# Optimization experiments

Measured on AMD Instinct MI355X. Metric: run time of the kernel, lower is better.

The kernel has to match this reference:

```python
import jax, jax.numpy as jnp
import numpy as np

# dims: T=tgt len, B=batch, S=src len, E=n_embed, H=n_hidden, V=vocab, L=n_layers
T, B, S, E, H, V, L = 64, 64, 256, 512, 1024, 16000, 2
PAD, SOS, EOS, COPY = 0, 1, 2, 3
EPS = 1e-7
NEG = -1e9  # additive mask for padded source positions


def setup_inputs() -> dict:
    key = jax.random.key(0)
    ks = jax.random.split(key, 16)
    r = lambda i, shape, s=0.02: jax.random.normal(ks[i], shape, jnp.float32) * s
    return dict(
        ref_tokens=jax.random.randint(ks[0], (T, B), 0, V),
        att_tokens=jax.random.randint(ks[1], (S, B), 0, V),
        att_features=jax.random.normal(ks[2], (S, B, H), jnp.float32),
        h0=jnp.zeros((L, B, H), jnp.float32),
        c0=jnp.zeros((L, B, H), jnp.float32),
        embed_w=r(3, (V, E)).at[PAD].set(0.0),  # padding_idx row zeroed
        W_ih0=r(4, (4 * H, E + H)), W_hh0=r(5, (4 * H, H)),
        b_ih0=r(6, (4 * H,), 0.01), b_hh0=r(7, (4 * H,), 0.01),
        W_ih1=r(8, (4 * H, H)), W_hh1=r(9, (4 * H, H)),
        b_ih1=r(10, (4 * H,), 0.01), b_hh1=r(11, (4 * H,), 0.01),
        Wk=r(12, (H, H)), bk=jnp.zeros(H, jnp.float32),
        Wq=r(13, (H, H)), bq=jnp.zeros(H, jnp.float32),
        Wc=r(14, (H, 2 * H)), bc=jnp.zeros(H, jnp.float32),
        Wp=r(15, (V, H)), bp=jnp.zeros(V, jnp.float32),
        Wsp=jax.random.normal(jax.random.fold_in(key, 99), (1, H), jnp.float32) * 0.02,
        bsp=jnp.zeros(1, jnp.float32),
    )


def _lstm_cell(x, h, c, W_ih, W_hh, b_ih, b_hh):
    # PyTorch gate order: i, f, g, o
    g = x @ W_ih.T + b_ih + h @ W_hh.T + b_hh
    i, f, gg, o = jnp.split(g, 4, axis=1)
    cn = jax.nn.sigmoid(f) * c + jax.nn.sigmoid(i) * jnp.tanh(gg)
    hn = jax.nn.sigmoid(o) * jnp.tanh(cn)
    return hn, cn


def reference(ref_tokens, att_tokens, att_features, h0, c0, embed_w,
              W_ih0, W_hh0, b_ih0, b_hh0, W_ih1, W_hh1, b_ih1, b_hh1,
              Wk, bk, Wq, bq, Wc, bc, Wp, bp, Wsp, bsp):
    mask = (att_tokens == PAD).astype(jnp.float32)              # (S,B)
    keys = jnp.einsum('sbh,kh->sbk', att_features, Wk) + bk     # (S,B,H), step-invariant
    bidx = jnp.broadcast_to(jnp.arange(B), (S, B))

    def step(carry, tok_t):
        feed, h, c = carry
        emb = embed_w[tok_t]                                    # (B,E)
        x = jnp.concatenate([emb, feed], axis=1)                # (B,E+H) concat_feed
        h0n, c0n = _lstm_cell(x, h[0], c[0], W_ih0, W_hh0, b_ih0, b_hh0)
        h1n, c1n = _lstm_cell(h0n, h[1], c[1], W_ih1, W_hh1, b_ih1, b_hh1)
        hidden = h1n                                            # (B,H) top layer
        # SimpleAttention: dot-product over time axis
        query = hidden @ Wq.T + bq
        scores = jnp.einsum('sbh,bh->sb', keys, query) + mask * NEG
        dist = jax.nn.softmax(scores, axis=0)                   # (S,B)
        summary = jnp.einsum('sb,sbh->bh', dist, att_features)
        comb = jnp.concatenate([hidden, summary], axis=1) @ Wc.T + bc  # (B,H)
        logits = comb @ Wp.T + bp                               # (B,V)
        probs = jax.nn.softmax(logits, axis=1)
        seq_probs = jax.nn.softmax(hidden @ Wsp.T + bsp, axis=1)  # (B,1) == 1 (single attn)
        wdist = dist * seq_probs[:, 0][None, :] * probs[:, COPY][None, :]  # (S,B)
        # one-hot projection matmul == scatter-add of weighted dist into token bins
        copy_probs = jnp.zeros((B, V), jnp.float32).at[bidx, att_tokens].add(wdist) + EPS
        comb_p = (copy_probs + probs).at[:, COPY].set(0.0)
        pred_logits = jnp.log(comb_p)                           # (B,V)
        return (comb, jnp.stack([h0n, h1n]), jnp.stack([c0n, c1n])), pred_logits

    feed0 = jnp.zeros((B, H), jnp.float32)
    _, preds = jax.lax.scan(step, (feed0, h0, c0), ref_tokens)
    return preds  # (T,B,V)
```

## Files before the change

kernel.cpp:

```cpp
#include <hip/hip_runtime.h>
#include <stdint.h>
#include <math.h>

#define Td 64
#define Bd 64
#define Sd 256
#define Ed 512
#define Hd 1024
#define Vd 16000
#define G4 4096

typedef short v8s __attribute__((ext_vector_type(8)));
typedef float v4f __attribute__((ext_vector_type(4)));

__device__ __forceinline__ float b2f(unsigned short v) {
  union { unsigned int u; float f; } x; x.u = ((unsigned int)v) << 16; return x.f;
}
__device__ __forceinline__ unsigned short f2b(float f) {
  union { float f; unsigned int u; } x; x.f = f;
  unsigned int u = x.u + 0x7fffu + ((x.u >> 16) & 1u);
  return (unsigned short)(u >> 16);
}


__global__ __launch_bounds__(256) void k_f2b(const float* __restrict__ s,
                                             unsigned short* __restrict__ d, int n) {
  int i = blockIdx.x * 256 + threadIdx.x;
  if (i < n) d[i] = f2b(s[i]);
}

__global__ __launch_bounds__(256) void k_cvtgate(const float* __restrict__ ih,
                                                 const float* __restrict__ hh,
                                                 unsigned short* __restrict__ dst,
                                                 int Kih, int Ktot) {
  int i = blockIdx.x * 256 + threadIdx.x;
  int np = i / Ktot;
  int k = i - np * Ktot;
  int n = ((np & 3) << 10) + (np >> 2);
  float v = (k < Kih) ? ih[(size_t)n * Kih + k]
                      : hh[(size_t)n * (Ktot - Kih) + (k - Kih)];
  dst[i] = f2b(v);
}

__global__ __launch_bounds__(256) void k_embed(const int* __restrict__ tok,
                                               const float* __restrict__ ew,
                                               unsigned short* __restrict__ dst) {
  int i = blockIdx.x * 256 + threadIdx.x;
  int e = i & (Ed - 1);
  int tb = i >> 9;
  dst[i] = f2b(ew[(size_t)tok[tb] * Ed + e]);
}

__global__ __launch_bounds__(256) void k_mt(const float* __restrict__ Wk,
                                            const float* __restrict__ Wq,
                                            unsigned short* __restrict__ MTT) {
  __shared__ float sk[32][33], sq[32][33];
  int tx = threadIdx.x & 15, ty = threadIdx.x >> 4;
  int n0 = blockIdx.x * 32, k0 = blockIdx.y * 32;
  float a00 = 0, a01 = 0, a10 = 0, a11 = 0;
  for (int jc = 0; jc < 32; jc++) {
    __syncthreads();
    for (int i = threadIdx.x; i < 1024; i += 256) {
      int r = i >> 5, c = i & 31;
      sk[r][c] = Wk[(jc * 32 + r) * Hd + n0 + c];
      sq[r][c] = Wq[(jc * 32 + r) * Hd + k0 + c];
    }
    __syncthreads();
    for (int j = 0; j < 32; j++) {
      float kv0 = sk[j][tx], kv1 = sk[j][tx + 16];
      float qv0 = sq[j][ty], qv1 = sq[j][ty + 16];
      a00 += kv0 * qv0; a01 += kv0 * qv1; a10 += kv1 * qv0; a11 += kv1 * qv1;
    }
  }
  MTT[(k0 + ty) * Hd + n0 + tx]             = f2b(a00);
  MTT[(k0 + ty + 16) * Hd + n0 + tx]        = f2b(a01);
  MTT[(k0 + ty) * Hd + n0 + tx + 16]        = f2b(a10);
  MTT[(k0 + ty + 16) * Hd + n0 + tx + 16]   = f2b(a11);
}

__global__ __launch_bounds__(256) void k_biasq(const float* __restrict__ bq,
                                               const float* __restrict__ Wk,
                                               float* __restrict__ biasq) {
  int n = blockIdx.x * 256 + threadIdx.x;
  float a = 0;
  for (int j = 0; j < 1024; j++) a += bq[j] * Wk[j * Hd + n];
  biasq[n] = a;
}

__global__ __launch_bounds__(256) void k_sb0(const unsigned short* __restrict__ Ab,
                                             const float* __restrict__ biasq,
                                             const int* __restrict__ atok,
                                             float* __restrict__ sb0) {
  int w = blockIdx.x * 4 + (threadIdx.x >> 6);
  int lane = threadIdx.x & 63;
  int s = w >> 6, b = w & 63;
  const unsigned short* ap = Ab + ((size_t)(s * 64 + b) << 10) + lane * 16;
  v8s a0 = *(const v8s*)ap, a1 = *(const v8s*)(ap + 8);
  float acc = 0;
#pragma unroll
  for (int j = 0; j < 8; j++) {
    acc += b2f((unsigned short)a0[j]) * biasq[lane * 16 + j];
    acc += b2f((unsigned short)a1[j]) * biasq[lane * 16 + 8 + j];
  }
  for (int off = 32; off; off >>= 1) acc += __shfl_xor(acc, off, 64);
  if (lane == 0) {
    if (atok[s * 64 + b] == 0) acc += -1e9f;
    sb0[s * 64 + b] = acc;
  }
}

__global__ __launch_bounds__(256) void k_bsum(const float* __restrict__ bih,
                                              const float* __restrict__ bhh,
                                              float* __restrict__ dst) {
  int i = blockIdx.x * 256 + threadIdx.x;
  int n = ((i & 3) << 10) + (i >> 2);
  dst[i] = bih[n] + bhh[n];
}

__global__ __launch_bounds__(256) void k_init(const float* __restrict__ h0in,
                                              const float* __restrict__ c0in,
                                              unsigned short* __restrict__ h0b,
                                              unsigned short* __restrict__ h1b,
                                              float* __restrict__ c0f, float* __restrict__ c1f,
                                              unsigned short* __restrict__ feed0) {
  int i = blockIdx.x * 256 + threadIdx.x;
  h0b[i] = f2b(h0in[i]);
  h1b[i] = f2b(h0in[Bd * Hd + i]);
  c0f[i] = c0in[i];
  c1f[i] = c0in[Bd * Hd + i];
  feed0[i] = 0;
}

struct GCArgs {
  const unsigned short *a0, *a1, *a2;
  int l0, l1, l2;
  const unsigned short* W; int ldw;
  int cpw;
  const float* bsum;
  float* c;
  unsigned short* hout;
  int mode;
};

__global__ __launch_bounds__(512) void k_gc(GCArgs g) {
  __shared__ float red[8][64][17];
  int tid = threadIdx.x;
  int w = tid >> 6, lane = tid & 63, lq = lane >> 4, l16 = lane & 15;
  int n0 = blockIdx.x * 16;
  int c0 = w * g.cpw;

  v4f acc[4];
#pragma unroll
  for (int mi = 0; mi < 4; mi++) acc[mi] = 0;

  auto ldA = [&](int ci, v8s af[4]) {
    int kv = (c0 + ci) * 32;
    const unsigned short* ap; int ld, ko;
    if (kv < g.l0) { ap = g.a0; ld = g.l0; ko = kv; }
    else if (kv < g.l0 + g.l1) { ap = g.a1; ld = g.l1; ko = kv - g.l0; }
    else { ap = g.a2; ld = g.l2; ko = kv - g.l0 - g.l1; }
    const unsigned short* base = ap + ko + lq * 8 + l16 * ld;
#pragma unroll
    for (int mi = 0; mi < 4; mi++) af[mi] = *(const v8s*)(base + mi * 16 * ld);
  };
  auto ldB = [&](int ci, v8s& bf) {
    bf = *(const v8s*)(g.W + (size_t)(n0 + l16) * g.ldw + (c0 + ci) * 32 + lq * 8);
  };

  v8s afc[4], afn[4], bfc, bfn;
  ldA(0, afc); ldB(0, bfc);
  for (int ci = 0; ci < g.cpw; ci++) {
    if (ci + 1 < g.cpw) { ldA(ci + 1, afn); ldB(ci + 1, bfn); }
#pragma unroll
    for (int mi = 0; mi < 4; mi++)
      acc[mi] = __builtin_amdgcn_mfma_f32_16x16x32_bf16(afc[mi], bfc, acc[mi], 0, 0, 0);
#pragma unroll
    for (int i = 0; i < 4; i++) afc[i] = afn[i];
    bfc = bfn;
  }

#pragma unroll
  for (int mi = 0; mi < 4; mi++)
#pragma unroll
    for (int r = 0; r < 4; r++)
      red[w][mi * 16 + lq * 4 + r][l16] = acc[mi][r];
  __syncthreads();

  if (g.mode == 0) {
    if (tid < 256) {
      int b = tid & 63, hl = tid >> 6;
      float gv[4];
#pragma unroll
      for (int gg = 0; gg < 4; gg++) {
        float s = g.bsum[n0 + hl * 4 + gg];
#pragma unroll
        for (int w8 = 0; w8 < 8; w8++) s += red[w8][b][hl * 4 + gg];
        gv[gg] = s;
      }
      float si = 1.f / (1.f + expf(-gv[0]));
      float sf = 1.f / (1.f + expf(-gv[1]));
      float so = 1.f / (1.f + expf(-gv[3]));
      int h = (n0 >> 2) + hl;
      int idx = (b << 10) + h;
      float cn = sf * g.c[idx] + si * tanhf(gv[2]);
      g.c[idx] = cn;
      g.hout[idx] = f2b(so * tanhf(cn));
    }
  } else {
    int b = tid & 63, nh = tid >> 6;
#pragma unroll
    for (int r = 0; r < 2; r++) {
      int nl = nh * 2 + r;
      float s = g.bsum[n0 + nl];
#pragma unroll
      for (int w8 = 0; w8 < 8; w8++) s += red[w8][b][nl];
      g.hout[(b << 10) + n0 + nl] = f2b(s);
    }
  }
}

__global__ __launch_bounds__(256) void k_scores(const unsigned short* __restrict__ AMT,
                                                const unsigned short* __restrict__ h1,
                                                const float* __restrict__ sb0,
                                                float* __restrict__ scores) {
  int w = blockIdx.x * 4 + (threadIdx.x >> 6);
  int lane = threadIdx.x & 63;
  int s = w >> 6, b = w & 63;
  const unsigned short* ap = AMT + ((size_t)(s * 64 + b) << 10) + lane * 16;
  const unsigned short* qp = h1 + (b << 10) + lane * 16;
  v8s a0 = *(const v8s*)ap, a1 = *(const v8s*)(ap + 8);
  v8s q0 = *(const v8s*)qp, q1 = *(const v8s*)(qp + 8);
  float acc = 0;
#pragma unroll
  for (int j = 0; j < 8; j++) {
    acc += b2f((unsigned short)a0[j]) * b2f((unsigned short)q0[j]);
    acc += b2f((unsigned short)a1[j]) * b2f((unsigned short)q1[j]);
  }
  for (int off = 32; off; off >>= 1) acc += __shfl_xor(acc, off, 64);
  if (lane == 0) scores[s * 64 + b] = acc + sb0[s * 64 + b];
}

__global__ __launch_bounds__(256) void k_ss(const float* __restrict__ scores,
                                            const unsigned short* __restrict__ Ab,
                                            float* __restrict__ dist_t,
                                            unsigned short* __restrict__ summb) {
  __shared__ float red[256];
  __shared__ float ds[256];
  int b = blockIdx.x >> 2, j = blockIdx.x & 3;
  int s = threadIdx.x;
  float x = scores[s * 64 + b];
  red[s] = x; __syncthreads();
  for (int off = 128; off; off >>= 1) { if (s < off) red[s] = fmaxf(red[s], red[s + off]); __syncthreads(); }
  float m = red[0];
  __syncthreads();
  float e = expf(x - m);
  red[s] = e; __syncthreads();
  for (int off = 128; off; off >>= 1) { if (s < off) red[s] += red[s + off]; __syncthreads(); }
  float d = e * (1.f / red[0]);
  ds[s] = d;
  if (j == 0) dist_t[b * 256 + s] = d;
  __syncthreads();
  int h = (j << 8) + s;
  const unsigned short* ap = Ab + ((size_t)b << 10) + h;
  float acc = 0;
  for (int s2 = 0; s2 < 256; s2++) acc += ds[s2] * b2f(ap[(size_t)s2 * 64 * Hd]);
  summb[b * Hd + h] = f2b(acc);
}

__global__ __launch_bounds__(256) void k_gemm_amt(const unsigned short* __restrict__ A,
                                                  const unsigned short* __restrict__ Bw,
                                                  unsigned short* __restrict__ C) {
  __shared__ unsigned short As[128 * 40], Bs[128 * 40];
  int tid = threadIdx.x;
  int mb = blockIdx.x * 128, nb = blockIdx.y * 128;
  int wv = tid >> 6, lane = tid & 63, lq = lane >> 4, l16 = lane & 15;
  int mo = (wv & 1) * 64, no = (wv >> 1) * 64;
  int srow = tid >> 1, sh = (tid & 1) * 16;
  v4f acc[4][4];
#pragma unroll
  for (int i = 0; i < 4; i++)
#pragma unroll
    for (int j = 0; j < 4; j++) acc[i][j] = 0;
  const unsigned short* gA = A + (size_t)(mb + srow) * Hd + sh;
  const unsigned short* gB = Bw + (size_t)(nb + srow) * Hd + sh;
  for (int kc = 0; kc < Hd / 32; kc++) {
    v8s a0 = *(const v8s*)(gA + kc * 32);
    v8s a1 = *(const v8s*)(gA + kc * 32 + 8);
    v8s b0 = *(const v8s*)(gB + kc * 32);
    v8s b1 = *(const v8s*)(gB + kc * 32 + 8);
    __syncthreads();
    *(v8s*)&As[srow * 40 + sh] = a0;
    *(v8s*)&As[srow * 40 + sh + 8] = a1;
    *(v8s*)&Bs[srow * 40 + sh] = b0;
    *(v8s*)&Bs[srow * 40 + sh + 8] = b1;
    __syncthreads();
    v8s af[4], bf[4];
#pragma unroll
    for (int i = 0; i < 4; i++) af[i] = *(const v8s*)&As[(mo + i * 16 + l16) * 40 + lq * 8];
#pragma unroll
    for (int j = 0; j < 4; j++) bf[j] = *(const v8s*)&Bs[(no + j * 16 + l16) * 40 + lq * 8];
#pragma unroll
    for (int i = 0; i < 4; i++)
#pragma unroll
      for (int j = 0; j < 4; j++)
        acc[i][j] = __builtin_amdgcn_mfma_f32_16x16x32_bf16(af[i], bf[j], acc[i][j], 0, 0, 0);
  }
#pragma unroll
  for (int i = 0; i < 4; i++)
#pragma unroll
    for (int j = 0; j < 4; j++)
#pragma unroll
      for (int r = 0; r < 4; r++) {
        int row = mb + mo + i * 16 + lq * 4 + r;
        int col = nb + no + j * 16 + l16;
        C[(size_t)row * Hd + col] = f2b(acc[i][j][r]);
      }
}

__global__ __launch_bounds__(256) void k_gemm_big(const unsigned short* __restrict__ A,
                                                  const unsigned short* __restrict__ Bw,
                                                  const float* __restrict__ bias,
                                                  float* __restrict__ C) {
  __shared__ unsigned short As[128 * 40], Bs[128 * 40];
  int tid = threadIdx.x;
  int mb = blockIdx.x * 128, nb = blockIdx.y * 128;
  int wv = tid >> 6, lane = tid & 63, lq = lane >> 4, l16 = lane & 15;
  int mo = (wv & 1) * 64, no = (wv >> 1) * 64;
  int srow = tid >> 1, sh = (tid & 1) * 16;
  v4f acc[4][4];
#pragma unroll
  for (int i = 0; i < 4; i++)
#pragma unroll
    for (int j = 0; j < 4; j++) acc[i][j] = 0;
  const unsigned short* gA = A + (size_t)(mb + srow) * Hd + sh;
  const unsigned short* gB = Bw + (size_t)(nb + srow) * Hd + sh;
  for (int kc = 0; kc < Hd / 32; kc++) {
    v8s a0 = *(const v8s*)(gA + kc * 32);
    v8s a1 = *(const v8s*)(gA + kc * 32 + 8);
    v8s b0 = *(const v8s*)(gB + kc * 32);
    v8s b1 = *(const v8s*)(gB + kc * 32 + 8);
    __syncthreads();
    *(v8s*)&As[srow * 40 + sh] = a0;
    *(v8s*)&As[srow * 40 + sh + 8] = a1;
    *(v8s*)&Bs[srow * 40 + sh] = b0;
    *(v8s*)&Bs[srow * 40 + sh + 8] = b1;
    __syncthreads();
    v8s af[4], bf[4];
#pragma unroll
    for (int i = 0; i < 4; i++) af[i] = *(const v8s*)&As[(mo + i * 16 + l16) * 40 + lq * 8];
#pragma unroll
    for (int j = 0; j < 4; j++) bf[j] = *(const v8s*)&Bs[(no + j * 16 + l16) * 40 + lq * 8];
#pragma unroll
    for (int i = 0; i < 4; i++)
#pragma unroll
      for (int j = 0; j < 4; j++)
        acc[i][j] = __builtin_amdgcn_mfma_f32_16x16x32_bf16(af[i], bf[j], acc[i][j], 0, 0, 0);
  }
#pragma unroll
  for (int i = 0; i < 4; i++)
#pragma unroll
    for (int j = 0; j < 4; j++)
#pragma unroll
      for (int r = 0; r < 4; r++) {
        int row = mb + mo + i * 16 + lq * 4 + r;
        int col = nb + no + j * 16 + l16;
        C[(size_t)row * Vd + col] = acc[i][j][r] + bias[col];
      }
}

#define VPT 32
__global__ __launch_bounds__(512) void k_epi(float* __restrict__ out,
                                             const float* __restrict__ distT,
                                             const int* __restrict__ atok) {
  __shared__ float bins[Vd];
  __shared__ float red[8];
  __shared__ float sh_e3;
  int row = blockIdx.x;
  int tid = threadIdx.x, w = tid >> 6, lane = tid & 63;
  float* p = out + (size_t)row * Vd;
  float ev[VPT];
  float mx = -1e30f;
#pragma unroll
  for (int j = 0; j < VPT; j++) {
    int col = j * 512 + tid;
    ev[j] = (col < Vd) ? p[col] : -1e30f;
    mx = fmaxf(mx, ev[j]);
  }
  for (int off = 32; off; off >>= 1) mx = fmaxf(mx, __shfl_xor(mx, off, 64));
  if (lane == 0) red[w] = mx;
  __syncthreads();
  float m = red[0];
#pragma unroll
  for (int i = 1; i < 8; i++) m = fmaxf(m, red[i]);
  __syncthreads();
  float sum = 0.f;
#pragma unroll
  for (int j = 0; j < VPT; j++) {
    int col = j * 512 + tid;
    float e = (col < Vd) ? expf(ev[j] - m) : 0.f;
    ev[j] = e;
    sum += e;
  }
  for (int off = 32; off; off >>= 1) sum += __shfl_xor(sum, off, 64);
  if (lane == 0) red[w] = sum;
  __syncthreads();
  float S = 0.f;
#pragma unroll
  for (int i = 0; i < 8; i++) S += red[i];
  if (tid == 3) sh_e3 = ev[0];
  for (int i = tid; i < Vd; i += 512) bins[i] = 0.f;
  __syncthreads();
  if (tid < 256) {
    int s = tid, b = row & 63;
    float wv = distT[(size_t)row * Sd + s] * sh_e3;
    atomicAdd(&bins[atok[s * 64 + b]], wv);
  }
  __syncthreads();
  float lS = logf(S);
  float eS = 1e-7f * S;
#pragma unroll
  for (int j = 0; j < VPT; j++) {
    int col = j * 512 + tid;
    if (col < Vd)
      p[col] = (col == 3) ? logf(1e-7f) : (logf(ev[j] + bins[col] + eS) - lS);
  }
}


extern "C" void kernel_launch(void* const* d_in, const int* in_sizes, int n_in,
                              void* d_out, int out_size, void* d_ws, size_t ws_size,
                              hipStream_t stream) {
  (void)in_sizes; (void)out_size;
  if (n_in < 22) return;
  const int* ref_tokens   = (const int*)d_in[0];
  const int* att_tokens   = (const int*)d_in[1];
  const float* att_feat   = (const float*)d_in[2];
  const float* h0in       = (const float*)d_in[3];
  const float* c0in       = (const float*)d_in[4];
  const float* embed_w    = (const float*)d_in[5];
  const float* W_ih0      = (const float*)d_in[6];
  const float* W_hh0      = (const float*)d_in[7];
  const float* b_ih0      = (const float*)d_in[8];
  const float* b_hh0      = (const float*)d_in[9];
  const float* W_ih1      = (const float*)d_in[10];
  const float* W_hh1      = (const float*)d_in[11];
  const float* b_ih1      = (const float*)d_in[12];
  const float* b_hh1      = (const float*)d_in[13];
  const float* Wk         = (const float*)d_in[14];
  const float* Wq         = (const float*)d_in[16];
  const float* bq         = (const float*)d_in[17];
  const float* Wc         = (const float*)d_in[18];
  const float* bc         = (const float*)d_in[19];
  const float* Wp         = (const float*)d_in[20];
  const float* bp         = (const float*)d_in[21];
  float* out = (float*)d_out;

  char* p = (char*)d_ws;
  auto alloc = [&](size_t bytes) -> char* {
    char* r = p; p += (bytes + 255) & ~(size_t)255; return r;
  };
  unsigned short* Wl0   = (unsigned short*)alloc((size_t)G4 * (Ed + 2 * Hd) * 2);
  unsigned short* Wl1   = (unsigned short*)alloc((size_t)G4 * 2 * Hd * 2);
  unsigned short* Wcb   = (unsigned short*)alloc((size_t)Hd * 2 * Hd * 2);
  unsigned short* Wpb   = (unsigned short*)alloc((size_t)Vd * Hd * 2);
  unsigned short* MTT   = (unsigned short*)alloc((size_t)Hd * Hd * 2);
  unsigned short* Aattb = (unsigned short*)alloc((size_t)Sd * Bd * Hd * 2);
  unsigned short* embb  = (unsigned short*)alloc((size_t)Td * Bd * Ed * 2);
  unsigned short* combb = (unsigned short*)alloc((size_t)Td * Bd * Hd * 2);
  float* distT          = (float*)alloc((size_t)Td * Bd * Sd * 4);
  float* sb0            = (float*)alloc((size_t)Sd * Bd * 4);
  float* biasq          = (float*)alloc((size_t)Hd * 4);
  float* bsum0          = (float*)alloc((size_t)G4 * 4);
  float* bsum1          = (float*)alloc((size_t)G4 * 4);
  unsigned short* h0buf[2];
  h0buf[0] = (unsigned short*)alloc((size_t)Bd * Hd * 2);
  h0buf[1] = (unsigned short*)alloc((size_t)Bd * Hd * 2);
  unsigned short* h1buf[2];
  h1buf[0] = (unsigned short*)alloc((size_t)Bd * Hd * 2);
  h1buf[1] = (unsigned short*)alloc((size_t)Bd * Hd * 2);
  float* c0f            = (float*)alloc((size_t)Bd * Hd * 4);
  float* c1f            = (float*)alloc((size_t)Bd * Hd * 4);
  unsigned short* feed0 = (unsigned short*)alloc((size_t)Bd * Hd * 2);
  float* scoresbuf      = (float*)alloc((size_t)Sd * Bd * 4);
  unsigned short* summb = (unsigned short*)alloc((size_t)Bd * Hd * 2);
  if ((size_t)(p - (char*)d_ws) > ws_size) return;

  unsigned short* AMTb = (unsigned short*)out;

  k_cvtgate<<<G4 * (Ed + 2 * Hd) / 256, 256, 0, stream>>>(W_ih0, W_hh0, Wl0, Ed + Hd, Ed + 2 * Hd);
  k_cvtgate<<<G4 * 2 * Hd / 256, 256, 0, stream>>>(W_ih1, W_hh1, Wl1, Hd, 2 * Hd);
  k_f2b<<<Hd * 2 * Hd / 256, 256, 0, stream>>>(Wc, Wcb, Hd * 2 * Hd);
  k_f2b<<<Vd * Hd / 256, 256, 0, stream>>>(Wp, Wpb, Vd * Hd);
  k_f2b<<<Sd * Bd * Hd / 256, 256, 0, stream>>>(att_feat, Aattb, Sd * Bd * Hd);
  k_embed<<<Td * Bd * Ed / 256, 256, 0, stream>>>(ref_tokens, embed_w, embb);
  k_mt<<<dim3(32, 32), 256, 0, stream>>>(Wk, Wq, MTT);
  k_biasq<<<4, 256, 0, stream>>>(bq, Wk, biasq);
  k_sb0<<<Sd * Bd / 4, 256, 0, stream>>>(Aattb, biasq, att_tokens, sb0);
  k_gemm_amt<<<dim3(Sd * Bd / 128, Hd / 128), 256, 0, stream>>>(Aattb, MTT, AMTb);
  k_bsum<<<16, 256, 0, stream>>>(b_ih0, b_hh0, bsum0);
  k_bsum<<<16, 256, 0, stream>>>(b_ih1, b_hh1, bsum1);
  k_init<<<Bd * Hd / 256, 256, 0, stream>>>(h0in, c0in, h0buf[0], h1buf[0], c0f, c1f, feed0);

  for (int t = 0; t < Td; t++) {
    int pr = t & 1;
    const unsigned short* emb_t = embb + (size_t)t * Bd * Ed;
    const unsigned short* feed = (t == 0) ? feed0 : combb + (size_t)(t - 1) * Bd * Hd;
    unsigned short* comb_t = combb + (size_t)t * Bd * Hd;
    float* dist_t = distT + (size_t)t * Bd * Sd;

    GCArgs g0{};
    g0.a0 = emb_t; g0.l0 = Ed; g0.a1 = feed; g0.l1 = Hd; g0.a2 = h0buf[pr]; g0.l2 = Hd;
    g0.W = Wl0; g0.ldw = Ed + 2 * Hd; g0.cpw = 10; g0.bsum = bsum0;
    g0.c = c0f; g0.hout = h0buf[1 - pr]; g0.mode = 0;
    k_gc<<<G4 / 16, 512, 0, stream>>>(g0);

    GCArgs g1{};
    g1.a0 = h0buf[1 - pr]; g1.l0 = Hd; g1.a1 = h1buf[pr]; g1.l1 = Hd;
    g1.a2 = h1buf[pr]; g1.l2 = Hd;
    g1.W = Wl1; g1.ldw = 2 * Hd; g1.cpw = 8; g1.bsum = bsum1;
    g1.c = c1f; g1.hout = h1buf[1 - pr]; g1.mode = 0;
    k_gc<<<G4 / 16, 512, 0, stream>>>(g1);

    k_scores<<<Sd * Bd / 4, 256, 0, stream>>>(AMTb, h1buf[1 - pr], sb0, scoresbuf);
    k_ss<<<Bd * 4, 256, 0, stream>>>(scoresbuf, Aattb, dist_t, summb);

    GCArgs gc{};
    gc.a0 = h1buf[1 - pr]; gc.l0 = Hd; gc.a1 = summb; gc.l1 = Hd;
    gc.a2 = summb; gc.l2 = Hd;
    gc.W = Wcb; gc.ldw = 2 * Hd; gc.cpw = 8; gc.bsum = bc;
    gc.c = nullptr; gc.hout = comb_t; gc.mode = 1;
    k_gc<<<Hd / 16, 512, 0, stream>>>(gc);
  }

  k_gemm_big<<<dim3(32, 125), 256, 0, stream>>>(combb, Wpb, bp, out);
  k_epi<<<Td * Bd, 512, 0, stream>>>(out, distT, att_tokens);
}
```

Baseline: 5.422 ms.

## Fuse recurrent timestep loop into persistent cooperative kernel with grid syncs

Replaces the per-timestep sequence of five kernel launches with one cooperative persistent kernel that loops over all timesteps and separates phases with grid-wide syncs. The scores, softmax and summary steps are merged into one block-per-batch attention phase. The combine GEMM is split so its hidden-state half runs alongside attention and writes a float partial, while the summary half finishes afterward. This removes about 320 launches and their gaps, at the cost of grid.sync overhead and lower per-phase parallelism, since attention now uses 128 blocks instead of many more. If the cooperative launch fails, a per-phase launch loop is used instead.

```diff
diff --git a/kernel.cpp b/kernel.cpp
--- a/kernel.cpp
+++ b/kernel.cpp
@@ -1,6 +1,9 @@
 #include <hip/hip_runtime.h>
+#include <hip/hip_cooperative_groups.h>
 #include <stdint.h>
 #include <math.h>
+
+namespace cg = cooperative_groups;
 
 #define Td 64
 #define Bd 64
@@ -131,23 +134,39 @@
   feed0[i] = 0;
 }
 
-struct GCArgs {
-  const unsigned short *a0, *a1, *a2;
-  int l0, l1, l2;
-  const unsigned short* W; int ldw;
-  int cpw;
-  const float* bsum;
-  float* c;
-  unsigned short* hout;
-  int mode;
+
+struct PK {
+  const unsigned short* embb;
+  const unsigned short* Wl0;
+  const unsigned short* Wl1;
+  const unsigned short* Wcb;
+  const unsigned short* AMT;
+  const unsigned short* Aatt;
+  const float* sb0;
+  const float* bsum0;
+  const float* bsum1;
+  const float* bc;
+  float* c0; float* c1;
+  unsigned short* h0[2];
+  unsigned short* h1[2];
+  const unsigned short* feed0;
+  unsigned short* combb;
+  float* distT;
+  unsigned short* summb;
+  float* cpart;
 };
 
-__global__ __launch_bounds__(512) void k_gc(GCArgs g) {
-  __shared__ float red[8][64][17];
-  int tid = threadIdx.x;
+__device__ __forceinline__ void gemm_phase(
+    int tid, int n0,
+    const unsigned short* a0, int l0,
+    const unsigned short* a1, int l1,
+    const unsigned short* a2, int l2,
+    const unsigned short* W, int ldw, int cpw,
+    const float* bsum, float* cst, unsigned short* hout,
+    float* cpart, const float* bc, int mode,
+    float (*red)[64][17]) {
   int w = tid >> 6, lane = tid & 63, lq = lane >> 4, l16 = lane & 15;
-  int n0 = blockIdx.x * 16;
-  int c0 = w * g.cpw;
+  int c0 = w * cpw;
 
   v4f acc[4];
 #pragma unroll
@@ -156,21 +175,21 @@
   auto ldA = [&](int ci, v8s af[4]) {
     int kv = (c0 + ci) * 32;
     const unsigned short* ap; int ld, ko;
-    if (kv < g.l0) { ap = g.a0; ld = g.l0; ko = kv; }
-    else if (kv < g.l0 + g.l1) { ap = g.a1; ld = g.l1; ko = kv - g.l0; }
-    else { ap = g.a2; ld = g.l2; ko = kv - g.l0 - g.l1; }
+    if (kv < l0) { ap = a0; ld = l0; ko = kv; }
+    else if (kv < l0 + l1) { ap = a1; ld = l1; ko = kv - l0; }
+    else { ap = a2; ld = l2; ko = kv - l0 - l1; }
     const unsigned short* base = ap + ko + lq * 8 + l16 * ld;
 #pragma unroll
     for (int mi = 0; mi < 4; mi++) af[mi] = *(const v8s*)(base + mi * 16 * ld);
   };
   auto ldB = [&](int ci, v8s& bf) {
-    bf = *(const v8s*)(g.W + (size_t)(n0 + l16) * g.ldw + (c0 + ci) * 32 + lq * 8);
+    bf = *(const v8s*)(W + (size_t)(n0 + l16) * ldw + (c0 + ci) * 32 + lq * 8);
   };
 
   v8s afc[4], afn[4], bfc, bfn;
   ldA(0, afc); ldB(0, bfc);
-  for (int ci = 0; ci < g.cpw; ci++) {
-    if (ci + 1 < g.cpw) { ldA(ci + 1, afn); ldB(ci + 1, bfn); }
+  for (int ci = 0; ci < cpw; ci++) {
+    if (ci + 1 < cpw) { ldA(ci + 1, afn); ldB(ci + 1, bfn); }
 #pragma unroll
     for (int mi = 0; mi < 4; mi++)
       acc[mi] = __builtin_amdgcn_mfma_f32_16x16x32_bf16(afc[mi], bfc, acc[mi], 0, 0, 0);
@@ -186,13 +205,13 @@
       red[w][mi * 16 + lq * 4 + r][l16] = acc[mi][r];
   __syncthreads();
 
-  if (g.mode == 0) {
+  if (mode == 0) {
     if (tid < 256) {
       int b = tid & 63, hl = tid >> 6;
       float gv[4];
 #pragma unroll
       for (int gg = 0; gg < 4; gg++) {
-        float s = g.bsum[n0 + hl * 4 + gg];
+        float s = bsum[n0 + hl * 4 + gg];
 #pragma unroll
         for (int w8 = 0; w8 < 8; w8++) s += red[w8][b][hl * 4 + gg];
         gv[gg] = s;
@@ -202,69 +221,133 @@
       float so = 1.f / (1.f + expf(-gv[3]));
       int h = (n0 >> 2) + hl;
       int idx = (b << 10) + h;
-      float cn = sf * g.c[idx] + si * tanhf(gv[2]);
-      g.c[idx] = cn;
-      g.hout[idx] = f2b(so * tanhf(cn));
+      float cn = sf * cst[idx] + si * tanhf(gv[2]);
+      cst[idx] = cn;
+      hout[idx] = f2b(so * tanhf(cn));
+    }
+  } else if (mode == 2) {
+    int b = tid & 63, nh = tid >> 6;
+#pragma unroll
+    for (int r = 0; r < 2; r++) {
+      int nl = nh * 2 + r;
+      float s = 0;
+#pragma unroll
+      for (int w8 = 0; w8 < 8; w8++) s += red[w8][b][nl];
+      cpart[(b << 10) + n0 + nl] = s;
     }
   } else {
     int b = tid & 63, nh = tid >> 6;
 #pragma unroll
     for (int r = 0; r < 2; r++) {
       int nl = nh * 2 + r;
-      float s = g.bsum[n0 + nl];
+      float s = cpart[(b << 10) + n0 + nl] + bc[n0 + nl];
 #pragma unroll
       for (int w8 = 0; w8 < 8; w8++) s += red[w8][b][nl];
-      g.hout[(b << 10) + n0 + nl] = f2b(s);
-    }
-  }
-}
-
-__global__ __launch_bounds__(256) void k_scores(const unsigned short* __restrict__ AMT,
-                                                const unsigned short* __restrict__ h1,
-                                                const float* __restrict__ sb0,
-                                                float* __restrict__ scores) {
-  int w = blockIdx.x * 4 + (threadIdx.x >> 6);
-  int lane = threadIdx.x & 63;
-  int s = w >> 6, b = w & 63;
-  const unsigned short* ap = AMT + ((size_t)(s * 64 + b) << 10) + lane * 16;
-  const unsigned short* qp = h1 + (b << 10) + lane * 16;
-  v8s a0 = *(const v8s*)ap, a1 = *(const v8s*)(ap + 8);
+      hout[(b << 10) + n0 + nl] = f2b(s);
+    }
+  }
+}
+
+__device__ __forceinline__ void att_phase(
+    int tid, int b, int half, int t, const PK& g, const unsigned short* h1n,
+    float* sc, float* ds) {
+  int w = tid >> 6, lane = tid & 63;
+  const unsigned short* qp = h1n + (b << 10) + lane * 16;
   v8s q0 = *(const v8s*)qp, q1 = *(const v8s*)(qp + 8);
+  for (int si = 0; si < 32; si++) {
+    int s = (w << 5) + si;
+    const unsigned short* ap = g.AMT + ((size_t)((s << 6) + b) << 10) + lane * 16;
+    v8s a0 = *(const v8s*)ap, a1 = *(const v8s*)(ap + 8);
+    float acc = 0;
+#pragma unroll
+    for (int j = 0; j < 8; j++) {
+      acc += b2f((unsigned short)a0[j]) * b2f((unsigned short)q0[j]);
+      acc += b2f((unsigned short)a1[j]) * b2f((unsigned short)q1[j]);
+    }
+    for (int off = 32; off; off >>= 1) acc += __shfl_xor(acc, off, 64);
+    if (lane == 0) sc[s] = acc + g.sb0[(s << 6) + b];
+  }
+  __syncthreads();
+  float x = (tid < 256) ? sc[tid] : -3e38f;
+  if (tid < 256) ds[tid] = x;
+  __syncthreads();
+  for (int off = 128; off; off >>= 1) {
+    if (tid < off) ds[tid] = fmaxf(ds[tid], ds[tid + off]);
+    __syncthreads();
+  }
+  float m = ds[0];
+  __syncthreads();
+  float e = (tid < 256) ? expf(x - m) : 0.f;
+  if (tid < 256) { sc[tid] = e; ds[tid] = e; }
+  __syncthreads();
+  for (int off = 128; off; off >>= 1) {
+    if (tid < off) ds[tid] += ds[tid + off];
+    __syncthreads();
+  }
+  float inv = 1.f / ds[0];
+  __syncthreads();
+  if (tid < 256) {
+    float d = sc[tid] * inv;
+    sc[tid] = d;
+    if (half == 0) g.distT[((size_t)((t << 6) + b) << 8) + tid] = d;
+  }
+  __syncthreads();
+  int h = (half << 9) + tid;
+  const unsigned short* ap = g.Aatt + ((size_t)b << 10) + h;
   float acc = 0;
-#pragma unroll
-  for (int j = 0; j < 8; j++) {
-    acc += b2f((unsigned short)a0[j]) * b2f((unsigned short)q0[j]);
-    acc += b2f((unsigned short)a1[j]) * b2f((unsigned short)q1[j]);
-  }
-  for (int off = 32; off; off >>= 1) acc += __shfl_xor(acc, off, 64);
-  if (lane == 0) scores[s * 64 + b] = acc + sb0[s * 64 + b];
-}
-
-__global__ __launch_bounds__(256) void k_ss(const float* __restrict__ scores,
-                                            const unsigned short* __restrict__ Ab,
-                                            float* __restrict__ dist_t,
-                                            unsigned short* __restrict__ summb) {
-  __shared__ float red[256];
+  for (int s2 = 0; s2 < 256; s2++) acc += sc[s2] * b2f(ap[(size_t)s2 << 16]);
+  g.summb[(b << 10) + h] = f2b(acc);
+}
+
+__device__ __forceinline__ void run_phase(const PK& g, int t, int ph, int bid, int tid,
+                                          float (*red)[64][17], float* sc, float* ds) {
+  int pr = t & 1;
+  if (ph == 0) {
+    const unsigned short* feed = (t == 0) ? g.feed0 : g.combb + ((size_t)(t - 1) << 16);
+    gemm_phase(tid, bid << 4, g.embb + ((size_t)t << 15), Ed, feed, Hd, g.h0[pr], Hd,
+               g.Wl0, Ed + 2 * Hd, 10, g.bsum0, g.c0, g.h0[1 - pr],
+               nullptr, nullptr, 0, red);
+  } else if (ph == 1) {
+    gemm_phase(tid, bid << 4, g.h0[1 - pr], Hd, g.h1[pr], Hd, g.h1[pr], Hd,
+               g.Wl1, 2 * Hd, 8, g.bsum1, g.c1, g.h1[1 - pr],
+               nullptr, nullptr, 0, red);
+  } else if (ph == 2) {
+    if (bid < 128) {
+      att_phase(tid, bid & 63, bid >> 6, t, g, g.h1[1 - pr], sc, ds);
+    } else if (bid < 192) {
+      gemm_phase(tid, (bid - 128) << 4, g.h1[1 - pr], Hd, g.h1[1 - pr], Hd,
+                 g.h1[1 - pr], Hd, g.Wcb, 2 * Hd, 4, nullptr, nullptr, nullptr,
+                 g.cpart, nullptr, 2, red);
+    }
+  } else {
+    if (bid < 64) {
+      gemm_phase(tid, bid << 4, g.summb, Hd, g.summb, Hd, g.summb, Hd,
+                 g.Wcb + Hd, 2 * Hd, 4, nullptr, nullptr,
+                 g.combb + ((size_t)t << 16), g.cpart, g.bc, 3, red);
+    }
+  }
+}
+
+__global__ __launch_bounds__(512) void k_recur(PK g) {
+  __shared__ float red[8][64][17];
+  __shared__ float sc[256];
   __shared__ float ds[256];
-  int b = blockIdx.x >> 2, j = blockIdx.x & 3;
-  int s = threadIdx.x;
-  float x = scores[s * 64 + b];
-  red[s] = x; __syncthreads();
-  for (int off = 128; off; off >>= 1) { if (s < off) red[s] = fmaxf(red[s], red[s + off]); __syncthreads(); }
-  float m = red[0];
-  __syncthreads();
-  float e = expf(x - m);
-  red[s] = e; __syncthreads();
-  for (int off = 128; off; off >>= 1) { if (s < off) red[s] += red[s + off]; __syncthreads(); }
-  float d = e * (1.f / red[0]);
-  ds[s] = d;
-  if (j == 0) dist_t[b * 256 + s] = d;
-  __syncthreads();
-  int h = (j << 8) + s;
-  const unsigned short* ap = Ab + ((size_t)b << 10) + h;
-  float acc = 0;
-  for (int s2 = 0; s2 < 256; s2++) acc += ds[s2] * b2f(ap[(size_t)s2 * 64 * Hd]);
-  summb[b * Hd + h] = f2b(acc);
+  cg::grid_group grid = cg::this_grid();
+  int bid = blockIdx.x, tid = threadIdx.x;
+  for (int t = 0; t < Td; t++) {
+#pragma unroll 1
+    for (int ph = 0; ph < 4; ph++) {
+      run_phase(g, t, ph, bid, tid, red, sc, ds);
+      grid.sync();
+    }
+  }
+}
+
+__global__ __launch_bounds__(512) void k_phase(PK g, int t, int ph) {
+  __shared__ float red[8][64][17];
+  __shared__ float sc[256];
+  __shared__ float ds[256];
+  run_phase(g, t, ph, blockIdx.x, threadIdx.x, red, sc, ds);
 }
 
 __global__ __launch_bounds__(256) void k_gemm_amt(const unsigned short* __restrict__ A,
@@ -472,17 +555,15 @@
   float* biasq          = (float*)alloc((size_t)Hd * 4);
   float* bsum0          = (float*)alloc((size_t)G4 * 4);
   float* bsum1          = (float*)alloc((size_t)G4 * 4);
-  unsigned short* h0buf[2];
-  h0buf[0] = (unsigned short*)alloc((size_t)Bd * Hd * 2);
-  h0buf[1] = (unsigned short*)alloc((size_t)Bd * Hd * 2);
-  unsigned short* h1buf[2];
-  h1buf[0] = (unsigned short*)alloc((size_t)Bd * Hd * 2);
-  h1buf[1] = (unsigned short*)alloc((size_t)Bd * Hd * 2);
+  unsigned short* h0a   = (unsigned short*)alloc((size_t)Bd * Hd * 2);
+  unsigned short* h0b2  = (unsigned short*)alloc((size_t)Bd * Hd * 2);
+  unsigned short* h1a   = (unsigned short*)alloc((size_t)Bd * Hd * 2);
+  unsigned short* h1b2  = (unsigned short*)alloc((size_t)Bd * Hd * 2);
   float* c0f            = (float*)alloc((size_t)Bd * Hd * 4);
   float* c1f            = (float*)alloc((size_t)Bd * Hd * 4);
   unsigned short* feed0 = (unsigned short*)alloc((size_t)Bd * Hd * 2);
-  float* scoresbuf      = (float*)alloc((size_t)Sd * Bd * 4);
   unsigned short* summb = (unsigned short*)alloc((size_t)Bd * Hd * 2);
+  float* cpart          = (float*)alloc((size_t)Bd * Hd * 4);
   if ((size_t)(p - (char*)d_ws) > ws_size) return;
 
   unsigned short* AMTb = (unsigned short*)out;
@@ -499,37 +580,28 @@
   k_gemm_amt<<<dim3(Sd * Bd / 128, Hd / 128), 256, 0, stream>>>(Aattb, MTT, AMTb);
   k_bsum<<<16, 256, 0, stream>>>(b_ih0, b_hh0, bsum0);
   k_bsum<<<16, 256, 0, stream>>>(b_ih1, b_hh1, bsum1);
-  k_init<<<Bd * Hd / 256, 256, 0, stream>>>(h0in, c0in, h0buf[0], h1buf[0], c0f, c1f, feed0);
-
-  for (int t = 0; t < Td; t++) {
-    int pr = t & 1;
-    const unsigned short* emb_t = embb + (size_t)t * Bd * Ed;
-    const unsigned short* feed = (t == 0) ? feed0 : combb + (size_t)(t - 1) * Bd * Hd;
-    unsigned short* comb_t = combb + (size_t)t * Bd * Hd;
-    float* dist_t = distT + (size_t)t * Bd * Sd;
-
-    GCArgs g0{};
-    g0.a0 = emb_t; g0.l0 = Ed; g0.a1 = feed; g0.l1 = Hd; g0.a2 = h0buf[pr]; g0.l2 = Hd;
-    g0.W = Wl0; g0.ldw = Ed + 2 * Hd; g0.cpw = 10; g0.bsum = bsum0;
-    g0.c = c0f; g0.hout = h0buf[1 - pr]; g0.mode = 0;
-    k_gc<<<G4 / 16, 512, 0, stream>>>(g0);
-
-    GCArgs g1{};
-    g1.a0 = h0buf[1 - pr]; g1.l0 = Hd; g1.a1 = h1buf[pr]; g1.l1 = Hd;
-    g1.a2 = h1buf[pr]; g1.l2 = Hd;
-    g1.W = Wl1; g1.ldw = 2 * Hd; g1.cpw = 8; g1.bsum = bsum1;
-    g1.c = c1f; g1.hout = h1buf[1 - pr]; g1.mode = 0;
-    k_gc<<<G4 / 16, 512, 0, stream>>>(g1);
-
-    k_scores<<<Sd * Bd / 4, 256, 0, stream>>>(AMTb, h1buf[1 - pr], sb0, scoresbuf);
-    k_ss<<<Bd * 4, 256, 0, stream>>>(scoresbuf, Aattb, dist_t, summb);
-
-    GCArgs gc{};
-    gc.a0 = h1buf[1 - pr]; gc.l0 = Hd; gc.a1 = summb; gc.l1 = Hd;
-    gc.a2 = summb; gc.l2 = Hd;
-    gc.W = Wcb; gc.ldw = 2 * Hd; gc.cpw = 8; gc.bsum = bc;
-    gc.c = nullptr; gc.hout = comb_t; gc.mode = 1;
-    k_gc<<<Hd / 16, 512, 0, stream>>>(gc);
+  k_init<<<Bd * Hd / 256, 256, 0, stream>>>(h0in, c0in, h0a, h1a, c0f, c1f, feed0);
+
+  PK pk{};
+  pk.embb = embb; pk.Wl0 = Wl0; pk.Wl1 = Wl1; pk.Wcb = Wcb;
+  pk.AMT = AMTb; pk.Aatt = Aattb; pk.sb0 = sb0;
+  pk.bsum0 = bsum0; pk.bsum1 = bsum1; pk.bc = bc;
+  pk.c0 = c0f; pk.c1 = c1f;
+  pk.h0[0] = h0a; pk.h0[1] = h0b2;
+  pk.h1[0] = h1a; pk.h1[1] = h1b2;
+  pk.feed0 = feed0; pk.combb = combb; pk.distT = distT;
+  pk.summb = summb; pk.cpart = cpart;
+
+  void* kargs[] = { (void*)&pk };
+  hipError_t ce = hipLaunchCooperativeKernel((const void*)k_recur, dim3(256), dim3(512),
+                                             kargs, 0, stream);
+  if (ce != hipSuccess) {
+    for (int t = 0; t < Td; t++) {
+      k_phase<<<256, 512, 0, stream>>>(pk, t, 0);
+      k_phase<<<256, 512, 0, stream>>>(pk, t, 1);
+      k_phase<<<192, 512, 0, stream>>>(pk, t, 2);
+      k_phase<<<64, 512, 0, stream>>>(pk, t, 3);
+    }
   }
 
   k_gemm_big<<<dim3(32, 125), 256, 0, stream>>>(combb, Wpb, bp, out);
```

New measurement: 13.44 ms. +147.9%, slower.
